# Kernel tuning notes

Hardware: AMD Instinct MI355X
Metric: run time of the kernel (lower is better)

Reference implementation:

```python
import jax, jax.numpy as jnp
import numpy as np

N = 100000
E = 600000
D_IN = 128
D_HID = 128
D_OUT = 128


def setup_inputs() -> dict:
    key = jax.random.key(0)
    k_x, k_e, k_w1, k_w2 = jax.random.split(key, 4)
    x = jax.random.normal(k_x, (N, D_IN), dtype=jnp.float32)
    edge_index = jax.random.randint(k_e, (2, E), 0, N, dtype=jnp.int64)
    # Glorot-ish init for the two GCN layers
    W1 = jax.random.normal(k_w1, (D_IN, D_HID), dtype=jnp.float32) / np.sqrt(D_IN)
    b1 = jnp.zeros((D_HID,), dtype=jnp.float32)
    W2 = jax.random.normal(k_w2, (D_HID, D_OUT), dtype=jnp.float32) / np.sqrt(D_HID)
    b2 = jnp.zeros((D_OUT,), dtype=jnp.float32)
    return {"x": x, "edge_index": edge_index, "W1": W1, "b1": b1, "W2": W2, "b2": b2}


def _gcn_layer(x, src, dst, deg_inv_sqrt, W, b, n_nodes):
    # out = D^-1/2 (A+I) D^-1/2 (x W) + b   (PyG GCNConv default)
    h = x @ W                                        # [N, D_out]
    norm = deg_inv_sqrt[src] * deg_inv_sqrt[dst]     # [E+N]
    msg = h[src] * norm[:, None]                     # gather + per-edge scale
    out = jax.ops.segment_sum(msg, dst, num_segments=n_nodes)
    return out + b


def reference(x, edge_index, W1, b1, W2, b2):
    n_nodes = x.shape[0]
    loops = jnp.arange(n_nodes, dtype=edge_index.dtype)
    src = jnp.concatenate([edge_index[0], loops])    # add self-loops
    dst = jnp.concatenate([edge_index[1], loops])
    deg = jax.ops.segment_sum(jnp.ones_like(src, dtype=x.dtype), dst,
                              num_segments=n_nodes)
    deg_inv_sqrt = jnp.where(deg > 0, jax.lax.rsqrt(deg), 0.0)
    h = _gcn_layer(x, src, dst, deg_inv_sqrt, W1, b1, n_nodes)
    h = jax.nn.relu(h)
    out = _gcn_layer(h, src, dst, deg_inv_sqrt, W2, b2, n_nodes)
    return out
```

## Files before the change

### kernel.cpp

```cpp
#include <hip/hip_runtime.h>


#define D 128

typedef __bf16 bf16x8 __attribute__((ext_vector_type(8)));
typedef float  f32x4  __attribute__((ext_vector_type(4)));

__global__ void k_zero_wprep(int* __restrict__ cnt, int n,
                             const float* __restrict__ W1, const float* __restrict__ W2,
                             __bf16* __restrict__ whi1, __bf16* __restrict__ wlo1,
                             __bf16* __restrict__ whi2, __bf16* __restrict__ wlo2) {
    int i = blockIdx.x * blockDim.x + threadIdx.x;
    if (i < n) cnt[i] = 0;
    if (i < 2 * D * D) {
        const float* W = (i < D * D) ? W1 : W2;
        __bf16* whi = (i < D * D) ? whi1 : whi2;
        __bf16* wlo = (i < D * D) ? wlo1 : wlo2;
        int ii = i & (D * D - 1);
        int k = ii >> 7, nn = ii & 127;
        float w = W[ii];
        __bf16 h = (__bf16)w;
        __bf16 l = (__bf16)(w - (float)h);
        int kt = k >> 5, kk = k & 31;
        int lane = (kk >> 3) * 16 + (nn & 15);
        int off = (((kt * 8) + (nn >> 4)) * 64 + lane) * 8 + (kk & 7);
        whi[off] = h;
        wlo[off] = l;
    }
}

__global__ __launch_bounds__(256) void k_histfill(const int* __restrict__ src,
                                                  const int* __restrict__ dst, int E,
                                                  int* __restrict__ cnt,
                                                  int* __restrict__ er) {
    int i = blockIdx.x * blockDim.x + threadIdx.x;
    if (i < E) {
        int d = dst[i];
        int s = src[i];
        int pos = atomicAdd(&cnt[d], 1);
        if (pos < 64) er[(size_t)d * 64 + pos] = s;
    }
}

__device__ inline void cvt_hilo(float4 v0, float4 v1, bf16x8& hi, bf16x8& lo) {
    float x[8] = {v0.x, v0.y, v0.z, v0.w, v1.x, v1.y, v1.z, v1.w};
#pragma unroll
    for (int j = 0; j < 8; ++j) {
        __bf16 h = (__bf16)x[j];
        hi[j] = h;
        lo[j] = (__bf16)(x[j] - (float)h);
    }
}

__global__ __launch_bounds__(256) void k_gemm1(const float* __restrict__ X,
                                               const __bf16* __restrict__ whi,
                                               const __bf16* __restrict__ wlo,
                                               const int* __restrict__ cnt,
                                               __bf16* __restrict__ G, int n) {
    const int tid = threadIdx.x;
    const int wid = tid >> 6;
    const int lane = tid & 63;
    const int lh = lane >> 4;
    const int lm = lane & 15;
    const int rowBase = blockIdx.x * 128 + wid * 32;

    bf16x8 ahi[2][4], alo[2][4];
#pragma unroll
    for (int mi = 0; mi < 2; ++mi) {
        int row = rowBase + mi * 16 + lm;
        if (row >= n) row = n - 1;
        const float* xp = X + (size_t)row * D + lh * 8;
#pragma unroll
        for (int kt = 0; kt < 4; ++kt) {
            float4 v0 = ((const float4*)(xp + kt * 32))[0];
            float4 v1 = ((const float4*)(xp + kt * 32))[1];
            cvt_hilo(v0, v1, ahi[mi][kt], alo[mi][kt]);
        }
    }

    f32x4 acc[2][8];
#pragma unroll
    for (int mi = 0; mi < 2; ++mi)
#pragma unroll
        for (int ni = 0; ni < 8; ++ni) acc[mi][ni] = (f32x4){0.f, 0.f, 0.f, 0.f};

#pragma unroll
    for (int kt = 0; kt < 4; ++kt) {
#pragma unroll
        for (int ni = 0; ni < 8; ++ni) {
            int foff = ((kt * 8 + ni) * 64 + lane) * 8;
            bf16x8 bh = *(const bf16x8*)(whi + foff);
            bf16x8 bl = *(const bf16x8*)(wlo + foff);
#pragma unroll
            for (int mi = 0; mi < 2; ++mi) {
                acc[mi][ni] = __builtin_amdgcn_mfma_f32_16x16x32_bf16(ahi[mi][kt], bh, acc[mi][ni], 0, 0, 0);
                acc[mi][ni] = __builtin_amdgcn_mfma_f32_16x16x32_bf16(alo[mi][kt], bh, acc[mi][ni], 0, 0, 0);
                acc[mi][ni] = __builtin_amdgcn_mfma_f32_16x16x32_bf16(ahi[mi][kt], bl, acc[mi][ni], 0, 0, 0);
            }
        }
    }

#pragma unroll
    for (int mi = 0; mi < 2; ++mi) {
        int r0 = rowBase + mi * 16 + (lane >> 4) * 4;
        int c = lane & 15;
#pragma unroll
        for (int r = 0; r < 4; ++r) {
            int row = r0 + r;
            if (row < n) {
                float scale = rsqrtf((float)(cnt[row] + 1));
#pragma unroll
                for (int ni = 0; ni < 8; ++ni)
                    G[(size_t)row * D + ni * 16 + c] = (__bf16)(acc[mi][ni][r] * scale);
            }
        }
    }
}

__global__ __launch_bounds__(256) void k_gemm2(const __bf16* __restrict__ X,
                                               const __bf16* __restrict__ whi,
                                               const __bf16* __restrict__ wlo,
                                               const int* __restrict__ cnt,
                                               __bf16* __restrict__ G, int n) {
    const int tid = threadIdx.x;
    const int wid = tid >> 6;
    const int lane = tid & 63;
    const int lh = lane >> 4;
    const int lm = lane & 15;
    const int rowBase = blockIdx.x * 128 + wid * 32;

    bf16x8 a[2][4];
#pragma unroll
    for (int mi = 0; mi < 2; ++mi) {
        int row = rowBase + mi * 16 + lm;
        if (row >= n) row = n - 1;
        const __bf16* xp = X + (size_t)row * D + lh * 8;
#pragma unroll
        for (int kt = 0; kt < 4; ++kt) a[mi][kt] = *(const bf16x8*)(xp + kt * 32);
    }

    f32x4 acc[2][8];
#pragma unroll
    for (int mi = 0; mi < 2; ++mi)
#pragma unroll
        for (int ni = 0; ni < 8; ++ni) acc[mi][ni] = (f32x4){0.f, 0.f, 0.f, 0.f};

#pragma unroll
    for (int kt = 0; kt < 4; ++kt) {
#pragma unroll
        for (int ni = 0; ni < 8; ++ni) {
            int foff = ((kt * 8 + ni) * 64 + lane) * 8;
            bf16x8 bh = *(const bf16x8*)(whi + foff);
            bf16x8 bl = *(const bf16x8*)(wlo + foff);
#pragma unroll
            for (int mi = 0; mi < 2; ++mi) {
                acc[mi][ni] = __builtin_amdgcn_mfma_f32_16x16x32_bf16(a[mi][kt], bh, acc[mi][ni], 0, 0, 0);
                acc[mi][ni] = __builtin_amdgcn_mfma_f32_16x16x32_bf16(a[mi][kt], bl, acc[mi][ni], 0, 0, 0);
            }
        }
    }

#pragma unroll
    for (int mi = 0; mi < 2; ++mi) {
        int r0 = rowBase + mi * 16 + (lane >> 4) * 4;
        int c = lane & 15;
#pragma unroll
        for (int r = 0; r < 4; ++r) {
            int row = r0 + r;
            if (row < n) {
                float scale = rsqrtf((float)(cnt[row] + 1));
#pragma unroll
                for (int ni = 0; ni < 8; ++ni)
                    G[(size_t)row * D + ni * 16 + c] = (__bf16)(acc[mi][ni][r] * scale);
            }
        }
    }
}

template <int RELU, int OUTBF>
__global__ __launch_bounds__(256) void k_agg(const __bf16* __restrict__ G,
                                             const int* __restrict__ cnt,
                                             const int* __restrict__ er,
                                             const float* __restrict__ bias,
                                             __bf16* __restrict__ outb,
                                             float* __restrict__ outf, int n) {
    int wave = threadIdx.x >> 6;
    int lane = threadIdx.x & 63;
    int node = blockIdx.x * 4 + wave;
    if (node >= n) return;
    int degTrue = cnt[node];
    float dn = rsqrtf((float)(degTrue + 1));
    int deg = degTrue > 64 ? 64 : degTrue;

    int s = 0;
    if (lane < deg) s = er[(size_t)node * 64 + lane];

    size_t nb = (size_t)node * D + lane * 2;
    unsigned selfpk = *(const unsigned*)(G + nb);
    float accx = __uint_as_float(selfpk << 16);
    float accy = __uint_as_float(selfpk & 0xffff0000u);

    for (int j0 = 0; j0 < deg; j0 += 8) {
#pragma unroll
        for (int u = 0; u < 8; ++u) {
            int j = j0 + u;
            int jc = j < 63 ? j : 63;
            int sj = __shfl(s, jc);
            float m = (j < deg) ? 1.0f : 0.0f;
            unsigned hv = *(const unsigned*)(G + (size_t)sj * D + lane * 2);
            accx += __uint_as_float(hv << 16) * m;
            accy += __uint_as_float(hv & 0xffff0000u) * m;
        }
    }
    float2 bv = *(const float2*)(bias + lane * 2);
    accx = accx * dn + bv.x;
    accy = accy * dn + bv.y;
    if (RELU) { accx = fmaxf(accx, 0.f); accy = fmaxf(accy, 0.f); }
    if (OUTBF) {
        __bf16 p0 = (__bf16)accx, p1 = (__bf16)accy;
        unsigned pk2 = ((unsigned)*(unsigned short*)&p1 << 16) | *(unsigned short*)&p0;
        *(unsigned*)(outb + nb) = pk2;
    } else {
        *(float2*)(outf + nb) = make_float2(accx, accy);
    }
}

extern "C" void kernel_launch(void* const* d_in, const int* in_sizes, int n_in,
                              void* d_out, int out_size, void* d_ws, size_t ws_size,
                              hipStream_t stream) {
    const float* x  = (const float*)d_in[0];
    const int*   ei = (const int*)d_in[1];
    const float* W1 = (const float*)d_in[2];
    const float* b1 = (const float*)d_in[3];
    const float* W2 = (const float*)d_in[4];
    const float* b2 = (const float*)d_in[5];
    float* out = (float*)d_out;

    const int N = in_sizes[0] / D;
    const int E = in_sizes[1] / 2;
    const int* srcv = ei;
    const int* dstv = ei + E;

    char* ws = (char*)d_ws;
    size_t off = 0;
    auto take = [&](size_t bytes) -> char* {
        char* p = ws + off;
        off += (bytes + 255) & ~(size_t)255;
        return p;
    };
    int*    cnt  = (int*)take((size_t)N * 4);
    int*    er   = (int*)take((size_t)N * 64 * 4);
    __bf16* whi1 = (__bf16*)take((size_t)D * D * 2);
    __bf16* wlo1 = (__bf16*)take((size_t)D * D * 2);
    __bf16* whi2 = (__bf16*)take((size_t)D * D * 2);
    __bf16* wlo2 = (__bf16*)take((size_t)D * D * 2);
    __bf16* hA   = (__bf16*)take((size_t)N * D * 2);
    __bf16* hB   = (__bf16*)take((size_t)N * D * 2);
    (void)ws_size; (void)n_in; (void)out_size;

    int zwBlocks = (N > 2 * D * D ? N : 2 * D * D);
    int eB = (E + 255) / 256;
    int gB = (N + 127) / 128;
    int aB = (N + 3) / 4;

    k_zero_wprep<<<(zwBlocks + 255) / 256, 256, 0, stream>>>(cnt, N, W1, W2,
                                                             whi1, wlo1, whi2, wlo2);
    k_histfill<<<eB, 256, 0, stream>>>(srcv, dstv, E, cnt, er);

    k_gemm1<<<gB, 256, 0, stream>>>(x, whi1, wlo1, cnt, hA, N);
    k_agg<1, 1><<<aB, 256, 0, stream>>>(hA, cnt, er, b1, hB, nullptr, N);
    k_gemm2<<<gB, 256, 0, stream>>>(hB, whi2, wlo2, cnt, hA, N);
    k_agg<0, 0><<<aB, 256, 0, stream>>>(hA, cnt, er, b2, nullptr, out, N);
}
```

Measured before the change: 164.1 us.

## Map each aggregation node to a 16-lane group with 16-byte vector gathers

```diff
diff --git a/kernel.cpp b/kernel.cpp
--- a/kernel.cpp
+++ b/kernel.cpp
@@ -5,6 +5,8 @@
 
 typedef __bf16 bf16x8 __attribute__((ext_vector_type(8)));
 typedef float  f32x4  __attribute__((ext_vector_type(4)));
+
+__device__ inline float b2f(unsigned u) { return __uint_as_float(u << 16); }
 
 __global__ void k_zero_wprep(int* __restrict__ cnt, int n,
                              const float* __restrict__ W1, const float* __restrict__ W2,
@@ -186,42 +188,71 @@
                                              float* __restrict__ outf, int n) {
     int wave = threadIdx.x >> 6;
     int lane = threadIdx.x & 63;
-    int node = blockIdx.x * 4 + wave;
+    int q = lane >> 4;
+    int l4 = lane & 15;
+    int node = blockIdx.x * 16 + wave * 4 + q;
     if (node >= n) return;
     int degTrue = cnt[node];
     float dn = rsqrtf((float)(degTrue + 1));
     int deg = degTrue > 64 ? 64 : degTrue;
 
-    int s = 0;
-    if (lane < deg) s = er[(size_t)node * 64 + lane];
-
-    size_t nb = (size_t)node * D + lane * 2;
-    unsigned selfpk = *(const unsigned*)(G + nb);
-    float accx = __uint_as_float(selfpk << 16);
-    float accy = __uint_as_float(selfpk & 0xffff0000u);
+    const int* bk = er + (size_t)node * 64;
+    int s0 = 0, s1 = 0, s2 = 0, s3 = 0;
+    if (l4 < deg)      s0 = bk[l4];
+    if (16 + l4 < deg) s1 = bk[16 + l4];
+    if (32 + l4 < deg) s2 = bk[32 + l4];
+    if (48 + l4 < deg) s3 = bk[48 + l4];
+
+    size_t nb = (size_t)node * D + l4 * 8;
+    uint4 sp = *(const uint4*)(G + nb);
+    float a0 = b2f(sp.x & 0xffffu), a1 = b2f(sp.x >> 16);
+    float a2 = b2f(sp.y & 0xffffu), a3 = b2f(sp.y >> 16);
+    float a4 = b2f(sp.z & 0xffffu), a5 = b2f(sp.z >> 16);
+    float a6 = b2f(sp.w & 0xffffu), a7 = b2f(sp.w >> 16);
 
     for (int j0 = 0; j0 < deg; j0 += 8) {
+        int sreg;
+        switch (j0 >> 4) {
+            case 0: sreg = s0; break;
+            case 1: sreg = s1; break;
+            case 2: sreg = s2; break;
+            default: sreg = s3; break;
+        }
 #pragma unroll
         for (int u = 0; u < 8; ++u) {
             int j = j0 + u;
-            int jc = j < 63 ? j : 63;
-            int sj = __shfl(s, jc);
+            int sj = __shfl(sreg, j & 15, 16);
             float m = (j < deg) ? 1.0f : 0.0f;
-            unsigned hv = *(const unsigned*)(G + (size_t)sj * D + lane * 2);
-            accx += __uint_as_float(hv << 16) * m;
-            accy += __uint_as_float(hv & 0xffff0000u) * m;
-        }
-    }
-    float2 bv = *(const float2*)(bias + lane * 2);
-    accx = accx * dn + bv.x;
-    accy = accy * dn + bv.y;
-    if (RELU) { accx = fmaxf(accx, 0.f); accy = fmaxf(accy, 0.f); }
+            uint4 hv = *(const uint4*)(G + (size_t)sj * D + l4 * 8);
+            a0 += b2f(hv.x & 0xffffu) * m;  a1 += b2f(hv.x >> 16) * m;
+            a2 += b2f(hv.y & 0xffffu) * m;  a3 += b2f(hv.y >> 16) * m;
+            a4 += b2f(hv.z & 0xffffu) * m;  a5 += b2f(hv.z >> 16) * m;
+            a6 += b2f(hv.w & 0xffffu) * m;  a7 += b2f(hv.w >> 16) * m;
+        }
+    }
+    float4 bv0 = *(const float4*)(bias + l4 * 8);
+    float4 bv1 = *(const float4*)(bias + l4 * 8 + 4);
+    a0 = a0 * dn + bv0.x;  a1 = a1 * dn + bv0.y;
+    a2 = a2 * dn + bv0.z;  a3 = a3 * dn + bv0.w;
+    a4 = a4 * dn + bv1.x;  a5 = a5 * dn + bv1.y;
+    a6 = a6 * dn + bv1.z;  a7 = a7 * dn + bv1.w;
+    if (RELU) {
+        a0 = fmaxf(a0, 0.f); a1 = fmaxf(a1, 0.f); a2 = fmaxf(a2, 0.f); a3 = fmaxf(a3, 0.f);
+        a4 = fmaxf(a4, 0.f); a5 = fmaxf(a5, 0.f); a6 = fmaxf(a6, 0.f); a7 = fmaxf(a7, 0.f);
+    }
     if (OUTBF) {
-        __bf16 p0 = (__bf16)accx, p1 = (__bf16)accy;
-        unsigned pk2 = ((unsigned)*(unsigned short*)&p1 << 16) | *(unsigned short*)&p0;
-        *(unsigned*)(outb + nb) = pk2;
+        __bf16 p0 = (__bf16)a0, p1 = (__bf16)a1, p2 = (__bf16)a2, p3 = (__bf16)a3;
+        __bf16 p4 = (__bf16)a4, p5 = (__bf16)a5, p6 = (__bf16)a6, p7 = (__bf16)a7;
+        uint4 pk;
+        pk.x = ((unsigned)*(unsigned short*)&p1 << 16) | *(unsigned short*)&p0;
+        pk.y = ((unsigned)*(unsigned short*)&p3 << 16) | *(unsigned short*)&p2;
+        pk.z = ((unsigned)*(unsigned short*)&p5 << 16) | *(unsigned short*)&p4;
+        pk.w = ((unsigned)*(unsigned short*)&p7 << 16) | *(unsigned short*)&p6;
+        *(uint4*)(outb + nb) = pk;
     } else {
-        *(float2*)(outf + nb) = make_float2(accx, accy);
+        float* op = outf + nb;
+        *(float4*)(op) = make_float4(a0, a1, a2, a3);
+        *(float4*)(op + 4) = make_float4(a4, a5, a6, a7);
     }
 }
 
@@ -261,7 +292,7 @@
     int zwBlocks = (N > 2 * D * D ? N : 2 * D * D);
     int eB = (E + 255) / 256;
     int gB = (N + 127) / 128;
-    int aB = (N + 3) / 4;
+    int aB = (N + 15) / 16;
 
     k_zero_wprep<<<(zwBlocks + 255) / 256, 256, 0, stream>>>(cnt, N, W1, W2,
                                                              whi1, wlo1, whi2, wlo2);
```

New measurement: 159.7 us. -2.6%, faster.
